# Optimization experiments

Measured on AMD Instinct MI355X. Metric: run time of the kernel, lower is better.

## Reference

```python
import jax, jax.numpy as jnp
import numpy as np

B, H, W, C = 2, 128, 128, 128
NS = 8                      # attn_num_splits
WH, WW = H // NS, W // NS   # window size 16x16
SH, SW = WH // 2, WW // 2   # shift sizes
HID = 2 * C * 4             # ffn hidden (in_channels = 2*d_model, expansion 4)
EPS = 1e-5


def _make_swin_mask():
    # Standard shifted-window attention mask: -100 between different regions.
    img = np.zeros((H, W), np.int32)
    cnt = 0
    for hs in (slice(0, -WH), slice(-WH, -SH), slice(-SH, None)):
        for ws in (slice(0, -WW), slice(-WW, -SW), slice(-SW, None)):
            img[hs, ws] = cnt
            cnt += 1
    ids = img.reshape(NS, WH, NS, WW).transpose(0, 2, 1, 3).reshape(NS * NS, WH * WW)
    mask = np.where(ids[:, None, :] != ids[:, :, None], -100.0, 0.0).astype(np.float32)
    return jnp.asarray(mask)  # (64, 256, 256)


def _layernorm(x, g, b):
    m = jnp.mean(x, axis=-1, keepdims=True)
    v = jnp.mean(jnp.square(x - m), axis=-1, keepdims=True)
    return (x - m) * jax.lax.rsqrt(v + EPS) * g + b


def setup_inputs() -> dict:
    key = jax.random.key(0)
    ks = jax.random.split(key, 8)
    s = 1.0 / np.sqrt(C)
    return {
        "source": jax.random.normal(ks[0], (B, H * W, C), jnp.float32),
        "target": jax.random.normal(ks[1], (B, H * W, C), jnp.float32),
        "Wq": jax.random.normal(ks[2], (C, C), jnp.float32) * s,
        "Wk": jax.random.normal(ks[3], (C, C), jnp.float32) * s,
        "Wv": jax.random.normal(ks[4], (C, C), jnp.float32) * s,
        "Wm": jax.random.normal(ks[5], (C, C), jnp.float32) * s,
        "g1": jnp.ones((C,), jnp.float32),
        "b1": jnp.zeros((C,), jnp.float32),
        "W1": jax.random.normal(ks[6], (2 * C, HID), jnp.float32) * (1.0 / np.sqrt(2 * C)),
        "W2": jax.random.normal(ks[7], (HID, C), jnp.float32) * (1.0 / np.sqrt(HID)),
        "g2": jnp.ones((C,), jnp.float32),
        "b2": jnp.zeros((C,), jnp.float32),
        "shifted_window_attn_mask": _make_swin_mask(),
        "height": H,
        "width": W,
        "attn_num_splits": NS,
    }


def reference(source, target, Wq, Wk, Wv, Wm, g1, b1, W1, W2, g2, b2,
              shifted_window_attn_mask, height, width, attn_num_splits):
    b, L, c = source.shape
    h, w, ns = height, width, attn_num_splits
    wh, ww = h // ns, w // ns
    sh, sw = wh // 2, ww // 2

    q = source @ Wq
    k = target @ Wk
    v = target @ Wv

    def to_windows(x):
        # (b, h*w, c) -> shifted -> (b, nWin, wh*ww, c)
        x = x.reshape(b, h, w, c)
        x = jnp.roll(x, (-sh, -sw), axis=(1, 2))
        x = x.reshape(b, ns, wh, ns, ww, c).transpose(0, 1, 3, 2, 4, 5)
        return x.reshape(b, ns * ns, wh * ww, c)

    qw, kw, vw = to_windows(q), to_windows(k), to_windows(v)
    scores = jnp.einsum('bnlc,bnmc->bnlm', qw, kw) / (c ** 0.5)
    scores = scores + shifted_window_attn_mask[None]  # broadcast over batch
    attn = jax.nn.softmax(scores, axis=-1)
    out = jnp.einsum('bnlm,bnmc->bnlc', attn, vw)

    # merge windows back and undo the shift
    out = out.reshape(b, ns, ns, wh, ww, c).transpose(0, 1, 3, 2, 4, 5).reshape(b, h, w, c)
    out = jnp.roll(out, (sh, sw), axis=(1, 2)).reshape(b, h * w, c)

    message = _layernorm(out @ Wm, g1, b1)
    ffn_in = jnp.concatenate([source, message], axis=-1)
    message = jax.nn.gelu(ffn_in @ W1, approximate=False) @ W2
    message = _layernorm(message, g2, b2)
    return source + message
```

## Files before the change

### kernel.cpp

```cpp
#include <hip/hip_runtime.h>
#include <math.h>
#include <stdint.h>


typedef unsigned short u16;
typedef __attribute__((ext_vector_type(8))) short bf16x8;
typedef __attribute__((ext_vector_type(4))) float f32x4;
typedef __attribute__((ext_vector_type(4))) short u16x4;
typedef __attribute__((ext_vector_type(2))) unsigned int u32x2;

__device__ __forceinline__ u16 f2b(float f) {
    unsigned int i = __float_as_uint(f);
    unsigned int r = (i + 0x7fffu + ((i >> 16) & 1u)) >> 16;
    return (u16)r;
}

__device__ __forceinline__ float gelu_e(float x) {
    float y = fabsf(x) * 0.70710678118f;
    float u = fmaf(y, fmaf(y, fmaf(y, fmaf(y, 0.078108f, 0.000972f),
                                   0.230389f), 0.278393f), 1.0f);
    u = u * u; u = u * u;
    float r = __builtin_amdgcn_rcpf(u);
    return fmaxf(x, 0.f) - 0.5f * fabsf(x) * r;
}

__device__ __forceinline__ void cp16(const void* g, void* l) {
    auto* gp = reinterpret_cast<const __attribute__((address_space(1))) unsigned int*>(
        reinterpret_cast<uintptr_t>(g));
    auto* lp = reinterpret_cast<__attribute__((address_space(3))) unsigned int*>(
        reinterpret_cast<uintptr_t>(l));
    __builtin_amdgcn_global_load_lds(gp, lp, 16, 0, 0);
}

__device__ __forceinline__ int win_map(int gm) {
    int b = gm >> 14, rr = gm & 16383;
    int win = rr >> 8, t = rr & 255;
    int wi = win >> 3, wj = win & 7, i = t >> 4, j = t & 15;
    int h = (wi * 16 + i + 8) & 127;
    int w = (wj * 16 + j + 8) & 127;
    return (b << 14) + h * 128 + w;
}

__global__ __launch_bounds__(256, 3)
void gemm_qkv(const u16* __restrict__ srcb, const u16* __restrict__ tgtb,
              const u16* __restrict__ Bt, u16* __restrict__ qw,
              u16* __restrict__ kw, u16* __restrict__ vwt)
{
    __shared__ __align__(16) u16 SMEM[17408];
    u16* Bs = SMEM;
    u16* Ts = SMEM;

    const int tid = threadIdx.x;
    const int w = tid >> 6, lane = tid & 63;
    const int lm = lane & 15, q = lane >> 4;
    const int wm = w >> 1, wn = w & 1;
    const int m0 = blockIdx.x * 128;
    const int y = blockIdx.y;
    const u16* Ab = (y == 0) ? srcb : tgtb;

#pragma unroll
    for (int s = 0; s < 4; ++s)
#pragma unroll
        for (int i = 0; i < 2; ++i) {
            int row = w * 32 + i * 16 + (lane >> 2);
            int kc = s * 32 + (lane & 3) * 8;
            cp16(Bt + (size_t)(y * 128 + row) * 128 + kc,
                 (void*)(Bs + (s * 128 + w * 32 + i * 16) * 32));
        }

    bf16x8 af[4][4];
#pragma unroll
    for (int t = 0; t < 4; ++t) {
        int row = win_map(m0 + wm * 64 + t * 16 + lm);
#pragma unroll
        for (int s = 0; s < 4; ++s)
            af[t][s] = *(const bf16x8*)(Ab + (size_t)row * 128 + s * 32 + q * 8);
    }
    __syncthreads();

    f32x4 acc[4][4] = {};
    __builtin_amdgcn_s_setprio(1);
#pragma unroll
    for (int s = 0; s < 4; ++s) {
        bf16x8 bfr[4];
#pragma unroll
        for (int t = 0; t < 4; ++t)
            bfr[t] = *(const bf16x8*)(Bs + (s * 128 + wn * 64 + t * 16 + lm) * 32 + q * 8);
#pragma unroll
        for (int mt = 0; mt < 4; ++mt)
#pragma unroll
            for (int nt = 0; nt < 4; ++nt)
                acc[mt][nt] = __builtin_amdgcn_mfma_f32_16x16x32_bf16(
                    af[mt][s], bfr[nt], acc[mt][nt], 0, 0, 0);
    }
    __builtin_amdgcn_s_setprio(0);

    __syncthreads();
#pragma unroll
    for (int mt = 0; mt < 4; ++mt)
#pragma unroll
        for (int nt = 0; nt < 4; ++nt)
#pragma unroll
            for (int r = 0; r < 4; ++r) {
                int rowl = wm * 64 + mt * 16 + q * 4 + r;
                int col = wn * 64 + nt * 16 + lm;
                int idx = (y == 2) ? col * 136 + rowl : rowl * 136 + col;
                Ts[idx] = f2b(acc[mt][nt][r]);
            }
    __syncthreads();
    const int c8 = (tid & 15) * 8;
#pragma unroll
    for (int i = 0; i < 8; ++i) {
        int rr = i * 16 + (tid >> 4);
        bf16x8 t = *(const bf16x8*)(Ts + rr * 136 + c8);
        if (y == 2) {
            int wix = m0 >> 8, tok0 = m0 & 255;
            *(bf16x8*)(vwt + (size_t)wix * 32768 + (size_t)rr * 256 + tok0 + c8) = t;
        } else {
            u16* Cv = (y == 0) ? qw : kw;
            *(bf16x8*)(Cv + (size_t)(m0 + rr) * 128 + c8) = t;
        }
    }
}

__global__ __launch_bounds__(256, 2)
void attn_msg(const u16* __restrict__ qw, const u16* __restrict__ kw,
              const u16* __restrict__ vt, const u16* __restrict__ wmt,
              const float* __restrict__ g, const float* __restrict__ bb,
              u16* __restrict__ msgb)
{
    __shared__ __align__(16) u16 Ps[64 * 264];
    __shared__ __align__(16) u16 B32[16384];

    const int tid = threadIdx.x, w = tid >> 6, lane = tid & 63;
    const int lm = lane & 15, q = lane >> 4;
    const int l4r = lane >> 2, l4c = (lane & 3) * 8;
    const int bid = blockIdx.x;
    const int qc = bid >> 7;
    const int gwin = bid & 127;
    const int win = gwin & 63, b = gwin >> 6;
    const int wi = win >> 3, wj = win & 7;
    const int q0 = qc * 64;
    const size_t wbase = (size_t)(b * 64 + win);
    const u16* kwb = kw + wbase * 256 * 128;
    const u16* qwb = qw + wbase * 256 * 128;
    const u16* vtb = vt + wbase * 128 * 256;

    u16* Qs = Ps;
#pragma unroll
    for (int i = 0; i < 4; ++i)
        cp16(qwb + (size_t)(q0 + w * 16 + l4r) * 128 + i * 32 + l4c,
             (void*)(Qs + (i * 64 + w * 16) * 32));
#pragma unroll
    for (int s = 0; s < 4; ++s)
#pragma unroll
        for (int i = 0; i < 2; ++i) {
            int tok = w * 32 + i * 16 + l4r;
            cp16(kwb + (size_t)tok * 128 + s * 32 + l4c,
                 (void*)(B32 + (s * 128 + w * 32 + i * 16) * 32));
        }
    __syncthreads();

    bf16x8 af[4];
#pragma unroll
    for (int kt = 0; kt < 4; ++kt)
        af[kt] = *(const bf16x8*)(Qs + (kt * 64 + w * 16 + lm) * 32 + q * 8);

    f32x4 s[16];
#pragma unroll
    for (int nt = 0; nt < 16; ++nt) { f32x4 z = {0.f, 0.f, 0.f, 0.f}; s[nt] = z; }
    __builtin_amdgcn_s_setprio(1);
#pragma unroll
    for (int kt = 0; kt < 4; ++kt)
#pragma unroll
        for (int nt = 0; nt < 8; ++nt) {
            bf16x8 bf = *(const bf16x8*)(B32 + (kt * 128 + nt * 16 + lm) * 32 + q * 8);
            s[nt] = __builtin_amdgcn_mfma_f32_16x16x32_bf16(af[kt], bf, s[nt], 0, 0, 0);
        }
    __builtin_amdgcn_s_setprio(0);
    __syncthreads();
#pragma unroll
    for (int ss = 0; ss < 4; ++ss)
#pragma unroll
        for (int i = 0; i < 2; ++i) {
            int tok = 128 + w * 32 + i * 16 + l4r;
            cp16(kwb + (size_t)tok * 128 + ss * 32 + l4c,
                 (void*)(B32 + (ss * 128 + w * 32 + i * 16) * 32));
        }
    __syncthreads();
    __builtin_amdgcn_s_setprio(1);
#pragma unroll
    for (int kt = 0; kt < 4; ++kt)
#pragma unroll
        for (int nt = 8; nt < 16; ++nt) {
            bf16x8 bf = *(const bf16x8*)(B32 + (kt * 128 + (nt - 8) * 16 + lm) * 32 + q * 8);
            s[nt] = __builtin_amdgcn_mfma_f32_16x16x32_bf16(af[kt], bf, s[nt], 0, 0, 0);
        }
    __builtin_amdgcn_s_setprio(0);
    __syncthreads();

#pragma unroll
    for (int tt = 0; tt < 4; ++tt)
#pragma unroll
        for (int i = 0; i < 2; ++i) {
            int ch = w * 32 + i * 16 + l4r;
            cp16(vtb + (size_t)ch * 256 + tt * 32 + l4c,
                 (void*)(B32 + (tt * 128 + w * 32 + i * 16) * 32));
        }

    int idk[16];
#pragma unroll
    for (int nt = 0; nt < 16; ++nt) {
        int rh = (wi == 7) ? ((nt >= 8) ? 2 : 1) : 0;
        int rw = (wj == 7) ? ((lm >= 8) ? 2 : 1) : 0;
        idk[nt] = rh * 3 + rw;
    }
    const float scale = 0.08838834764831845f;
#pragma unroll
    for (int r = 0; r < 4; ++r) {
        int tq = q0 + w * 16 + q * 4 + r;
        int iq = tq >> 4, jq = tq & 15;
        int rhq = (wi == 7) ? ((iq >= 8) ? 2 : 1) : 0;
        int rwq = (wj == 7) ? ((jq >= 8) ? 2 : 1) : 0;
        int idq = rhq * 3 + rwq;
        float sv[16];
        float mx = -1e30f;
#pragma unroll
        for (int nt = 0; nt < 16; ++nt) {
            float x = s[nt][r] * scale + ((idq != idk[nt]) ? -100.f : 0.f);
            sv[nt] = x; mx = fmaxf(mx, x);
        }
        mx = fmaxf(mx, __shfl_xor(mx, 1));
        mx = fmaxf(mx, __shfl_xor(mx, 2));
        mx = fmaxf(mx, __shfl_xor(mx, 4));
        mx = fmaxf(mx, __shfl_xor(mx, 8));
        float sum = 0.f;
#pragma unroll
        for (int nt = 0; nt < 16; ++nt) { float e = __expf(sv[nt] - mx); sv[nt] = e; sum += e; }
        sum += __shfl_xor(sum, 1);
        sum += __shfl_xor(sum, 2);
        sum += __shfl_xor(sum, 4);
        sum += __shfl_xor(sum, 8);
        float inv = 1.0f / sum;
#pragma unroll
        for (int nt = 0; nt < 16; ++nt)
            Ps[(w * 16 + q * 4 + r) * 264 + nt * 16 + lm] = f2b(sv[nt] * inv);
    }
    __syncthreads();

    f32x4 o[8];
#pragma unroll
    for (int nt = 0; nt < 8; ++nt) { f32x4 z = {0.f, 0.f, 0.f, 0.f}; o[nt] = z; }
    __builtin_amdgcn_s_setprio(1);
#pragma unroll
    for (int tt = 0; tt < 4; ++tt) {
        bf16x8 pf = *(const bf16x8*)(Ps + (w * 16 + lm) * 264 + tt * 32 + q * 8);
#pragma unroll
        for (int nt = 0; nt < 8; ++nt) {
            bf16x8 vf = *(const bf16x8*)(B32 + (tt * 128 + nt * 16 + lm) * 32 + q * 8);
            o[nt] = __builtin_amdgcn_mfma_f32_16x16x32_bf16(pf, vf, o[nt], 0, 0, 0);
        }
    }
    __builtin_amdgcn_s_setprio(0);
    __syncthreads();
#pragma unroll
    for (int tt = 0; tt < 4; ++tt)
#pragma unroll
        for (int i = 0; i < 2; ++i) {
            int ch = w * 32 + i * 16 + l4r;
            cp16(vtb + (size_t)ch * 256 + 128 + tt * 32 + l4c,
                 (void*)(B32 + (tt * 128 + w * 32 + i * 16) * 32));
        }
    __syncthreads();
    __builtin_amdgcn_s_setprio(1);
#pragma unroll
    for (int tt = 4; tt < 8; ++tt) {
        bf16x8 pf = *(const bf16x8*)(Ps + (w * 16 + lm) * 264 + tt * 32 + q * 8);
#pragma unroll
        for (int nt = 0; nt < 8; ++nt) {
            bf16x8 vf = *(const bf16x8*)(B32 + ((tt - 4) * 128 + nt * 16 + lm) * 32 + q * 8);
            o[nt] = __builtin_amdgcn_mfma_f32_16x16x32_bf16(pf, vf, o[nt], 0, 0, 0);
        }
    }
    __builtin_amdgcn_s_setprio(0);
    __syncthreads();

#pragma unroll
    for (int ss = 0; ss < 4; ++ss)
#pragma unroll
        for (int i = 0; i < 2; ++i) {
            int n = w * 32 + i * 16 + l4r;
            cp16(wmt + (size_t)n * 128 + ss * 32 + l4c,
                 (void*)(B32 + (ss * 128 + w * 32 + i * 16) * 32));
        }
    u16* Ot = Ps;
#pragma unroll
    for (int r = 0; r < 4; ++r) {
        int rl = w * 16 + q * 4 + r;
#pragma unroll
        for (int nt = 0; nt < 8; ++nt)
            Ot[rl * 136 + nt * 16 + lm] = f2b(o[nt][r]);
    }
    __syncthreads();

    f32x4 macc[8];
#pragma unroll
    for (int n2 = 0; n2 < 8; ++n2) { f32x4 z = {0.f, 0.f, 0.f, 0.f}; macc[n2] = z; }
    __builtin_amdgcn_s_setprio(1);
#pragma unroll
    for (int kt = 0; kt < 4; ++kt) {
        bf16x8 paf = *(const bf16x8*)(Ot + (w * 16 + lm) * 136 + kt * 32 + q * 8);
#pragma unroll
        for (int n2 = 0; n2 < 8; ++n2) {
            bf16x8 wf = *(const bf16x8*)(B32 + (kt * 128 + n2 * 16 + lm) * 32 + q * 8);
            macc[n2] = __builtin_amdgcn_mfma_f32_16x16x32_bf16(paf, wf, macc[n2], 0, 0, 0);
        }
    }
    __builtin_amdgcn_s_setprio(0);

    float gv[8], bv[8];
#pragma unroll
    for (int n2 = 0; n2 < 8; ++n2) {
        int col = n2 * 16 + lm;
        gv[n2] = g[col]; bv[n2] = bb[col];
    }
#pragma unroll
    for (int r = 0; r < 4; ++r) {
        float s1 = 0.f, s2 = 0.f;
#pragma unroll
        for (int n2 = 0; n2 < 8; ++n2) {
            float v = macc[n2][r];
            s1 += v; s2 += v * v;
        }
        s1 += __shfl_xor(s1, 1); s2 += __shfl_xor(s2, 1);
        s1 += __shfl_xor(s1, 2); s2 += __shfl_xor(s2, 2);
        s1 += __shfl_xor(s1, 4); s2 += __shfl_xor(s2, 4);
        s1 += __shfl_xor(s1, 8); s2 += __shfl_xor(s2, 8);
        float mean = s1 * (1.f / 128.f);
        float var = fmaxf(s2 * (1.f / 128.f) - mean * mean, 0.f);
        float rs = rsqrtf(var + 1e-5f);
        int t = q0 + w * 16 + q * 4 + r;
        int ii = t >> 4, jj = t & 15;
        int h = (wi * 16 + ii + 8) & 127;
        int w2 = (wj * 16 + jj + 8) & 127;
        size_t orow = ((size_t)b * 16384 + h * 128 + w2) * 128;
#pragma unroll
        for (int n2 = 0; n2 < 8; ++n2)
            msgb[orow + n2 * 16 + lm] = f2b((macc[n2][r] - mean) * rs * gv[n2] + bv[n2]);
    }
}

__global__ __launch_bounds__(512, 4)
void fused_ffn(const u16* __restrict__ A0, const u16* __restrict__ A1,
               const u16* __restrict__ W1T, const u16* __restrict__ W2T,
               const float* __restrict__ g, const float* __restrict__ bb,
               const float* __restrict__ resid, float* __restrict__ outv)
{
    __shared__ __align__(16) u16 W1s[16384];
    __shared__ __align__(16) u16 W2s[16384];
    __shared__ __align__(16) u16 Gs[4096];

    const int tid = threadIdx.x;
    const int w = tid >> 6, lane = tid & 63;
    const int lm = lane & 15, q = lane >> 4;
    const int l4r = lane >> 2, l4c = (lane & 3) * 8;
    const int wm = w >> 2, wn = w & 3;
    const int m0 = blockIdx.x * 64;

    const u16* w1p = W1T + (size_t)l4r * 256 + w * 32 + l4c;
    const u16* w2p = W2T + (size_t)((w & 3) * 32 + l4r) * 1024 + (w >> 2) * 32 + l4c;
    u16* const w1d = W1s + (w * 64) * 32;
    u16* const w2d0 = W2s + (((w >> 2) * 128 + (w & 3) * 32)) * 32;
    u16* const w2d1 = w2d0 + 8192;

    bf16x8 areg[2][8];
#pragma unroll
    for (int mt = 0; mt < 2; ++mt)
#pragma unroll
        for (int ks = 0; ks < 8; ++ks) {
            const u16* Ab = (ks < 4) ? A0 : A1;
            areg[mt][ks] = *(const bf16x8*)(
                Ab + (size_t)(m0 + wm * 32 + mt * 16 + lm) * 128 + (ks & 3) * 32 + q * 8);
        }

#pragma unroll
    for (int i = 0; i < 4; ++i)
        cp16(w1p + (size_t)(i * 16) * 256, w1d + (i * 16) * 32);
#pragma unroll
    for (int i = 0; i < 2; ++i)
        cp16(w2p + (size_t)(i * 16) * 1024, w2d0 + (i * 16) * 32);
    w1p += 16384; w2p += 64;
    __syncthreads();

    f32x4 acc2[2][2] = {};
#pragma unroll 2
    for (int c = 0; c < 16; ++c) {
        const int cb = c & 1, nb = cb ^ 1;

        {
            f32x4 acc1[2] = {};
            __builtin_amdgcn_s_setprio(1);
#pragma unroll
            for (int ks = 0; ks < 8; ++ks) {
                bf16x8 w1f = *(const bf16x8*)(W1s + (ks * 64 + wn * 16 + lm) * 32 + q * 8);
#pragma unroll
                for (int mt = 0; mt < 2; ++mt)
                    acc1[mt] = __builtin_amdgcn_mfma_f32_16x16x32_bf16(
                        w1f, areg[mt][ks], acc1[mt], 0, 0, 0);
            }
            __builtin_amdgcn_s_setprio(0);
#pragma unroll
            for (int mt = 0; mt < 2; ++mt) {
                float g0 = gelu_e(acc1[mt][0]), g1 = gelu_e(acc1[mt][1]);
                float g2 = gelu_e(acc1[mt][2]), g3 = gelu_e(acc1[mt][3]);
                unsigned p0, p1;
                asm("v_cvt_pk_bf16_f32 %0, %1, %2" : "=v"(p0) : "v"(g0), "v"(g1));
                asm("v_cvt_pk_bf16_f32 %0, %1, %2" : "=v"(p1) : "v"(g2), "v"(g3));
                int tok = wm * 32 + mt * 16 + lm;
                int slot = (wn * 2 + (q >> 1)) ^ (tok & 7);
                u32x2 pk; pk[0] = p0; pk[1] = p1;
                *(u32x2*)(Gs + tok * 64 + slot * 8 + (q & 1) * 4) = pk;
            }
        }
        __syncthreads();

        if (c + 1 < 16) {
#pragma unroll
            for (int i = 0; i < 4; ++i)
                cp16(w1p + (size_t)(i * 16) * 256, w1d + (i * 16) * 32);
            u16* d = nb ? w2d1 : w2d0;
#pragma unroll
            for (int i = 0; i < 2; ++i)
                cp16(w2p + (size_t)(i * 16) * 1024, d + (i * 16) * 32);
        }
        w1p += 16384; w2p += 64;

        {
            const u16* W2c = W2s + cb * 8192;
            __builtin_amdgcn_s_setprio(1);
#pragma unroll
            for (int ks = 0; ks < 2; ++ks) {
                bf16x8 pa[2], wf[2];
#pragma unroll
                for (int mt = 0; mt < 2; ++mt) {
                    int tok = wm * 32 + mt * 16 + lm;
                    pa[mt] = *(const bf16x8*)(Gs + tok * 64 + (((ks * 4 + q) ^ (tok & 7)) * 8));
                }
#pragma unroll
                for (int nt = 0; nt < 2; ++nt)
                    wf[nt] = *(const bf16x8*)(W2c + (ks * 128 + wn * 32 + nt * 16 + lm) * 32 + q * 8);
#pragma unroll
                for (int mt = 0; mt < 2; ++mt)
#pragma unroll
                    for (int nt = 0; nt < 2; ++nt)
                        acc2[mt][nt] = __builtin_amdgcn_mfma_f32_16x16x32_bf16(
                            pa[mt], wf[nt], acc2[mt][nt], 0, 0, 0);
            }
            __builtin_amdgcn_s_setprio(0);
        }
        __syncthreads();
    }

    float* stats = (float*)Gs;
#pragma unroll
    for (int mt = 0; mt < 2; ++mt)
#pragma unroll
        for (int r = 0; r < 4; ++r) {
            float s1 = 0.f, s2 = 0.f;
#pragma unroll
            for (int nt = 0; nt < 2; ++nt) {
                float v = acc2[mt][nt][r];
                s1 += v; s2 += v * v;
            }
            s1 += __shfl_xor(s1, 1); s2 += __shfl_xor(s2, 1);
            s1 += __shfl_xor(s1, 2); s2 += __shfl_xor(s2, 2);
            s1 += __shfl_xor(s1, 4); s2 += __shfl_xor(s2, 4);
            s1 += __shfl_xor(s1, 8); s2 += __shfl_xor(s2, 8);
            if (lm == 0) {
                int row = wm * 32 + mt * 16 + q * 4 + r;
                stats[row * 8 + wn * 2] = s1;
                stats[row * 8 + wn * 2 + 1] = s2;
            }
        }
    __syncthreads();

    float gv[2], bv[2];
#pragma unroll
    for (int nt = 0; nt < 2; ++nt) {
        int col = wn * 32 + nt * 16 + lm;
        gv[nt] = g[col]; bv[nt] = bb[col];
    }
#pragma unroll
    for (int mt = 0; mt < 2; ++mt)
#pragma unroll
        for (int r = 0; r < 4; ++r) {
            int row = wm * 32 + mt * 16 + q * 4 + r;
            f32x4 st0 = *(const f32x4*)(stats + row * 8);
            f32x4 st1 = *(const f32x4*)(stats + row * 8 + 4);
            float s1 = st0[0] + st0[2] + st1[0] + st1[2];
            float s2 = st0[1] + st0[3] + st1[1] + st1[3];
            float mean = s1 * (1.f / 128.f);
            float var = fmaxf(s2 * (1.f / 128.f) - mean * mean, 0.f);
            float rs = rsqrtf(var + 1e-5f);
#pragma unroll
            for (int nt = 0; nt < 2; ++nt) {
                int col = wn * 32 + nt * 16 + lm;
                size_t gi = (size_t)(m0 + row) * 128 + col;
                outv[gi] = (acc2[mt][nt][r] - mean) * rs * gv[nt] + bv[nt] + resid[gi];
            }
        }
}

__global__ void prep_all(const float* __restrict__ Wq, const float* __restrict__ Wk,
                         const float* __restrict__ Wv, const float* __restrict__ Wm,
                         const float* __restrict__ W1, const float* __restrict__ W2,
                         const float* __restrict__ src, const float* __restrict__ tgt,
                         u16* __restrict__ ws, u16* __restrict__ srcb,
                         u16* __restrict__ tgtb)
{
    int bx = blockIdx.x;
    if (bx < 112) {
        __shared__ float T[64][65];
        const int t = threadIdx.x;
        const float* sp; u16* dst; int R, C, r0, c0;
        if (bx < 16) {
            int m = bx >> 2, tt = bx & 3;
            sp = (m == 0) ? Wq : (m == 1) ? Wk : (m == 2) ? Wv : Wm;
            R = 128; C = 128; r0 = (tt >> 1) * 64; c0 = (tt & 1) * 64;
            dst = ws + m * 16384;
        } else if (bx < 80) {
            int tt = bx - 16;
            sp = W1; R = 256; C = 1024;
            r0 = (tt >> 4) * 64; c0 = (tt & 15) * 64;
            dst = ws + 65536;
        } else {
            int tt = bx - 80;
            sp = W2; R = 1024; C = 128;
            r0 = (tt >> 1) * 64; c0 = (tt & 1) * 64;
            dst = ws + 327680;
        }
#pragma unroll
        for (int i = 0; i < 16; ++i) {
            int idx = i * 256 + t, r = idx >> 6, c = idx & 63;
            T[r][c] = sp[(size_t)(r0 + r) * C + c0 + c];
        }
        __syncthreads();
#pragma unroll
        for (int i = 0; i < 16; ++i) {
            int idx = i * 256 + t, n = idx >> 6, k = idx & 63;
            dst[(size_t)(c0 + n) * R + r0 + k] = f2b(T[k][n]);
        }
    } else {
        int idx = (bx - 112) * 256 + threadIdx.x;
        const float* s; u16* d; int i;
        if (idx < 1048576) { s = src; d = srcb; i = idx * 4; }
        else               { s = tgt; d = tgtb; i = (idx - 1048576) * 4; }
        f32x4 v = *(const f32x4*)(s + i);
        u16x4 o; o[0] = f2b(v[0]); o[1] = f2b(v[1]); o[2] = f2b(v[2]); o[3] = f2b(v[3]);
        *(u16x4*)(d + i) = o;
    }
}

#define OFF_WQT  0u
#define OFF_WMT  49152u
#define OFF_W1T  65536u
#define OFF_W2T  327680u
#define OFF_SRCB 458752u
#define OFF_TGTB 4653056u
#define OFF_QW   8847360u
#define OFF_KW   13041664u
#define OFF_VWT  17235968u
#define OFF_MSGB 21430272u

extern "C" void kernel_launch(void* const* d_in, const int* in_sizes, int n_in,
                              void* d_out, int out_size, void* d_ws, size_t ws_size,
                              hipStream_t stream)
{
    (void)in_sizes; (void)n_in; (void)out_size; (void)ws_size;
    const float* source = (const float*)d_in[0];
    const float* target = (const float*)d_in[1];
    const float* Wq = (const float*)d_in[2];
    const float* Wk = (const float*)d_in[3];
    const float* Wv = (const float*)d_in[4];
    const float* Wm = (const float*)d_in[5];
    const float* g1 = (const float*)d_in[6];
    const float* b1 = (const float*)d_in[7];
    const float* W1 = (const float*)d_in[8];
    const float* W2 = (const float*)d_in[9];
    const float* g2 = (const float*)d_in[10];
    const float* b2 = (const float*)d_in[11];
    u16* ws = (u16*)d_ws;
    float* out = (float*)d_out;

    prep_all<<<8304, 256, 0, stream>>>(Wq, Wk, Wv, Wm, W1, W2, source, target,
                                       ws, ws + OFF_SRCB, ws + OFF_TGTB);
    gemm_qkv<<<dim3(256, 3), 256, 0, stream>>>(
        ws + OFF_SRCB, ws + OFF_TGTB, ws + OFF_WQT,
        ws + OFF_QW, ws + OFF_KW, ws + OFF_VWT);
    attn_msg<<<512, 256, 0, stream>>>(
        ws + OFF_QW, ws + OFF_KW, ws + OFF_VWT, ws + OFF_WMT, g1, b1,
        ws + OFF_MSGB);
    fused_ffn<<<512, 512, 0, stream>>>(
        ws + OFF_SRCB, ws + OFF_MSGB, ws + OFF_W1T, ws + OFF_W2T,
        g2, b2, source, out);
}
```

Measured before the change: 186.4 us.

## Fuse fp32-to-bf16 input conversion into GEMM loads and double-buffer K tiles

```diff
diff --git a/kernel.cpp b/kernel.cpp
--- a/kernel.cpp
+++ b/kernel.cpp
@@ -13,6 +13,15 @@
     unsigned int i = __float_as_uint(f);
     unsigned int r = (i + 0x7fffu + ((i >> 16) & 1u)) >> 16;
     return (u16)r;
+}
+
+__device__ __forceinline__ bf16x8 pk8(f32x4 a, f32x4 b) {
+    union { bf16x8 v; unsigned u[4]; } r;
+    asm("v_cvt_pk_bf16_f32 %0, %1, %2" : "=v"(r.u[0]) : "v"(a[0]), "v"(a[1]));
+    asm("v_cvt_pk_bf16_f32 %0, %1, %2" : "=v"(r.u[1]) : "v"(a[2]), "v"(a[3]));
+    asm("v_cvt_pk_bf16_f32 %0, %1, %2" : "=v"(r.u[2]) : "v"(b[0]), "v"(b[1]));
+    asm("v_cvt_pk_bf16_f32 %0, %1, %2" : "=v"(r.u[3]) : "v"(b[2]), "v"(b[3]));
+    return r.v;
 }
 
 __device__ __forceinline__ float gelu_e(float x) {
@@ -42,7 +51,7 @@
 }
 
 __global__ __launch_bounds__(256, 3)
-void gemm_qkv(const u16* __restrict__ srcb, const u16* __restrict__ tgtb,
+void gemm_qkv(const float* __restrict__ srcf, const float* __restrict__ tgtf,
               const u16* __restrict__ Bt, u16* __restrict__ qw,
               u16* __restrict__ kw, u16* __restrict__ vwt)
 {
@@ -56,7 +65,7 @@
     const int wm = w >> 1, wn = w & 1;
     const int m0 = blockIdx.x * 128;
     const int y = blockIdx.y;
-    const u16* Ab = (y == 0) ? srcb : tgtb;
+    const float* Af = (y == 0) ? srcf : tgtf;
 
 #pragma unroll
     for (int s = 0; s < 4; ++s)
@@ -71,10 +80,13 @@
     bf16x8 af[4][4];
 #pragma unroll
     for (int t = 0; t < 4; ++t) {
-        int row = win_map(m0 + wm * 64 + t * 16 + lm);
-#pragma unroll
-        for (int s = 0; s < 4; ++s)
-            af[t][s] = *(const bf16x8*)(Ab + (size_t)row * 128 + s * 32 + q * 8);
+        const float* ap = Af + (size_t)win_map(m0 + wm * 64 + t * 16 + lm) * 128;
+#pragma unroll
+        for (int s = 0; s < 4; ++s) {
+            f32x4 a = *(const f32x4*)(ap + s * 32 + q * 8);
+            f32x4 b = *(const f32x4*)(ap + s * 32 + q * 8 + 4);
+            af[t][s] = pk8(a, b);
+        }
     }
     __syncthreads();
 
@@ -165,35 +177,26 @@
 #pragma unroll
     for (int kt = 0; kt < 4; ++kt)
         af[kt] = *(const bf16x8*)(Qs + (kt * 64 + w * 16 + lm) * 32 + q * 8);
-
-    f32x4 s[16];
-#pragma unroll
-    for (int nt = 0; nt < 16; ++nt) { f32x4 z = {0.f, 0.f, 0.f, 0.f}; s[nt] = z; }
-    __builtin_amdgcn_s_setprio(1);
-#pragma unroll
-    for (int kt = 0; kt < 4; ++kt)
-#pragma unroll
-        for (int nt = 0; nt < 8; ++nt) {
-            bf16x8 bf = *(const bf16x8*)(B32 + (kt * 128 + nt * 16 + lm) * 32 + q * 8);
-            s[nt] = __builtin_amdgcn_mfma_f32_16x16x32_bf16(af[kt], bf, s[nt], 0, 0, 0);
-        }
-    __builtin_amdgcn_s_setprio(0);
-    __syncthreads();
+    __syncthreads();
+
 #pragma unroll
     for (int ss = 0; ss < 4; ++ss)
 #pragma unroll
         for (int i = 0; i < 2; ++i) {
             int tok = 128 + w * 32 + i * 16 + l4r;
             cp16(kwb + (size_t)tok * 128 + ss * 32 + l4c,
-                 (void*)(B32 + (ss * 128 + w * 32 + i * 16) * 32));
-        }
-    __syncthreads();
+                 (void*)(Ps + (ss * 128 + w * 32 + i * 16) * 32));
+        }
+
+    f32x4 s[16];
+#pragma unroll
+    for (int nt = 0; nt < 16; ++nt) { f32x4 z = {0.f, 0.f, 0.f, 0.f}; s[nt] = z; }
     __builtin_amdgcn_s_setprio(1);
 #pragma unroll
     for (int kt = 0; kt < 4; ++kt)
 #pragma unroll
-        for (int nt = 8; nt < 16; ++nt) {
-            bf16x8 bf = *(const bf16x8*)(B32 + (kt * 128 + (nt - 8) * 16 + lm) * 32 + q * 8);
+        for (int nt = 0; nt < 8; ++nt) {
+            bf16x8 bf = *(const bf16x8*)(B32 + (kt * 128 + nt * 16 + lm) * 32 + q * 8);
             s[nt] = __builtin_amdgcn_mfma_f32_16x16x32_bf16(af[kt], bf, s[nt], 0, 0, 0);
         }
     __builtin_amdgcn_s_setprio(0);
@@ -207,6 +210,16 @@
             cp16(vtb + (size_t)ch * 256 + tt * 32 + l4c,
                  (void*)(B32 + (tt * 128 + w * 32 + i * 16) * 32));
         }
+    __builtin_amdgcn_s_setprio(1);
+#pragma unroll
+    for (int kt = 0; kt < 4; ++kt)
+#pragma unroll
+        for (int nt = 8; nt < 16; ++nt) {
+            bf16x8 bf = *(const bf16x8*)(Ps + (kt * 128 + (nt - 8) * 16 + lm) * 32 + q * 8);
+            s[nt] = __builtin_amdgcn_mfma_f32_16x16x32_bf16(af[kt], bf, s[nt], 0, 0, 0);
+        }
+    __builtin_amdgcn_s_setprio(0);
+    __syncthreads();
 
     int idk[16];
 #pragma unroll
@@ -246,7 +259,6 @@
         for (int nt = 0; nt < 16; ++nt)
             Ps[(w * 16 + q * 4 + r) * 264 + nt * 16 + lm] = f2b(sv[nt] * inv);
     }
-    __syncthreads();
 
     f32x4 o[8];
 #pragma unroll
@@ -351,7 +363,7 @@
 }
 
 __global__ __launch_bounds__(512, 4)
-void fused_ffn(const u16* __restrict__ A0, const u16* __restrict__ A1,
+void fused_ffn(const float* __restrict__ A0f, const u16* __restrict__ A1,
                const u16* __restrict__ W1T, const u16* __restrict__ W2T,
                const float* __restrict__ g, const float* __restrict__ bb,
                const float* __restrict__ resid, float* __restrict__ outv)
@@ -375,13 +387,20 @@
 
     bf16x8 areg[2][8];
 #pragma unroll
-    for (int mt = 0; mt < 2; ++mt)
-#pragma unroll
-        for (int ks = 0; ks < 8; ++ks) {
-            const u16* Ab = (ks < 4) ? A0 : A1;
+    for (int mt = 0; mt < 2; ++mt) {
+        const int row = m0 + wm * 32 + mt * 16 + lm;
+        const float* ap = A0f + (size_t)row * 128;
+#pragma unroll
+        for (int ks = 0; ks < 4; ++ks) {
+            f32x4 a = *(const f32x4*)(ap + ks * 32 + q * 8);
+            f32x4 b = *(const f32x4*)(ap + ks * 32 + q * 8 + 4);
+            areg[mt][ks] = pk8(a, b);
+        }
+#pragma unroll
+        for (int ks = 4; ks < 8; ++ks)
             areg[mt][ks] = *(const bf16x8*)(
-                Ab + (size_t)(m0 + wm * 32 + mt * 16 + lm) * 128 + (ks & 3) * 32 + q * 8);
-        }
+                A1 + (size_t)row * 128 + (ks & 3) * 32 + q * 8);
+    }
 
 #pragma unroll
     for (int i = 0; i < 4; ++i)
@@ -514,50 +533,38 @@
 __global__ void prep_all(const float* __restrict__ Wq, const float* __restrict__ Wk,
                          const float* __restrict__ Wv, const float* __restrict__ Wm,
                          const float* __restrict__ W1, const float* __restrict__ W2,
-                         const float* __restrict__ src, const float* __restrict__ tgt,
-                         u16* __restrict__ ws, u16* __restrict__ srcb,
-                         u16* __restrict__ tgtb)
+                         u16* __restrict__ ws)
 {
+    __shared__ float T[64][65];
     int bx = blockIdx.x;
-    if (bx < 112) {
-        __shared__ float T[64][65];
-        const int t = threadIdx.x;
-        const float* sp; u16* dst; int R, C, r0, c0;
-        if (bx < 16) {
-            int m = bx >> 2, tt = bx & 3;
-            sp = (m == 0) ? Wq : (m == 1) ? Wk : (m == 2) ? Wv : Wm;
-            R = 128; C = 128; r0 = (tt >> 1) * 64; c0 = (tt & 1) * 64;
-            dst = ws + m * 16384;
-        } else if (bx < 80) {
-            int tt = bx - 16;
-            sp = W1; R = 256; C = 1024;
-            r0 = (tt >> 4) * 64; c0 = (tt & 15) * 64;
-            dst = ws + 65536;
-        } else {
-            int tt = bx - 80;
-            sp = W2; R = 1024; C = 128;
-            r0 = (tt >> 1) * 64; c0 = (tt & 1) * 64;
-            dst = ws + 327680;
-        }
-#pragma unroll
-        for (int i = 0; i < 16; ++i) {
-            int idx = i * 256 + t, r = idx >> 6, c = idx & 63;
-            T[r][c] = sp[(size_t)(r0 + r) * C + c0 + c];
-        }
-        __syncthreads();
-#pragma unroll
-        for (int i = 0; i < 16; ++i) {
-            int idx = i * 256 + t, n = idx >> 6, k = idx & 63;
-            dst[(size_t)(c0 + n) * R + r0 + k] = f2b(T[k][n]);
-        }
+    const int t = threadIdx.x;
+    const float* sp; u16* dst; int R, C, r0, c0;
+    if (bx < 16) {
+        int m = bx >> 2, tt = bx & 3;
+        sp = (m == 0) ? Wq : (m == 1) ? Wk : (m == 2) ? Wv : Wm;
+        R = 128; C = 128; r0 = (tt >> 1) * 64; c0 = (tt & 1) * 64;
+        dst = ws + m * 16384;
+    } else if (bx < 80) {
+        int tt = bx - 16;
+        sp = W1; R = 256; C = 1024;
+        r0 = (tt >> 4) * 64; c0 = (tt & 15) * 64;
+        dst = ws + 65536;
     } else {
-        int idx = (bx - 112) * 256 + threadIdx.x;
-        const float* s; u16* d; int i;
-        if (idx < 1048576) { s = src; d = srcb; i = idx * 4; }
-        else               { s = tgt; d = tgtb; i = (idx - 1048576) * 4; }
-        f32x4 v = *(const f32x4*)(s + i);
-        u16x4 o; o[0] = f2b(v[0]); o[1] = f2b(v[1]); o[2] = f2b(v[2]); o[3] = f2b(v[3]);
-        *(u16x4*)(d + i) = o;
+        int tt = bx - 80;
+        sp = W2; R = 1024; C = 128;
+        r0 = (tt >> 1) * 64; c0 = (tt & 1) * 64;
+        dst = ws + 327680;
+    }
+#pragma unroll
+    for (int i = 0; i < 16; ++i) {
+        int idx = i * 256 + t, r = idx >> 6, c = idx & 63;
+        T[r][c] = sp[(size_t)(r0 + r) * C + c0 + c];
+    }
+    __syncthreads();
+#pragma unroll
+    for (int i = 0; i < 16; ++i) {
+        int idx = i * 256 + t, n = idx >> 6, k = idx & 63;
+        dst[(size_t)(c0 + n) * R + r0 + k] = f2b(T[k][n]);
     }
 }
 
@@ -565,12 +572,10 @@
 #define OFF_WMT  49152u
 #define OFF_W1T  65536u
 #define OFF_W2T  327680u
-#define OFF_SRCB 458752u
-#define OFF_TGTB 4653056u
-#define OFF_QW   8847360u
-#define OFF_KW   13041664u
-#define OFF_VWT  17235968u
-#define OFF_MSGB 21430272u
+#define OFF_QW   458752u
+#define OFF_KW   4653056u
+#define OFF_VWT  8847360u
+#define OFF_MSGB 13041664u
 
 extern "C" void kernel_launch(void* const* d_in, const int* in_sizes, int n_in,
                               void* d_out, int out_size, void* d_ws, size_t ws_size,
@@ -592,15 +597,14 @@
     u16* ws = (u16*)d_ws;
     float* out = (float*)d_out;
 
-    prep_all<<<8304, 256, 0, stream>>>(Wq, Wk, Wv, Wm, W1, W2, source, target,
-                                       ws, ws + OFF_SRCB, ws + OFF_TGTB);
+    prep_all<<<112, 256, 0, stream>>>(Wq, Wk, Wv, Wm, W1, W2, ws);
     gemm_qkv<<<dim3(256, 3), 256, 0, stream>>>(
-        ws + OFF_SRCB, ws + OFF_TGTB, ws + OFF_WQT,
+        source, target, ws + OFF_WQT,
         ws + OFF_QW, ws + OFF_KW, ws + OFF_VWT);
     attn_msg<<<512, 256, 0, stream>>>(
         ws + OFF_QW, ws + OFF_KW, ws + OFF_VWT, ws + OFF_WMT, g1, b1,
         ws + OFF_MSGB);
     fused_ffn<<<512, 512, 0, stream>>>(
-        ws + OFF_SRCB, ws + OFF_MSGB, ws + OFF_W1T, ws + OFF_W2T,
+        source, ws + OFF_MSGB, ws + OFF_W1T, ws + OFF_W2T,
         g2, b2, source, out);
 }
```

Result: no change. 187.3 us (+0.5%).
